# Optimization experiments

Measured on AMD Instinct MI355X. Metric: run time of the kernel, lower is better.

The kernel has to match this reference:

```python
import jax, jax.numpy as jnp
import numpy as np

N_HEADS, N_KV, HEAD_DIM = 16, 4, 64
DIM = 4096
LATENT = N_HEADS * HEAD_DIM   # 1024
KV_DIM = N_KV * HEAD_DIM      # 256
KSZ = 3


def _causal_conv1d(x, w, b, groups):
    # x: [B,S,C]; w: [Cout, Cin//groups, K]; causal left padding (K-1)
    y = jax.lax.conv_general_dilated(
        x.transpose(0, 2, 1), w, window_strides=(1,),
        padding=[(w.shape[-1] - 1, 0)], feature_group_count=groups,
        dimension_numbers=('NCH', 'OIH', 'NCH'))
    return (y + b[None, :, None]).transpose(0, 2, 1)


def _rope(x, cos, sin):
    # x: [B,H,S,D] interleaved pairs; cos/sin: [1,1,S,D//2]
    x1, x2 = x[..., ::2], x[..., 1::2]
    out = jnp.stack([x1 * cos - x2 * sin, x1 * sin + x2 * cos], axis=-1)
    return out.reshape(x.shape)


def _l2norm(x):
    n = jnp.sqrt(jnp.sum(x * x, axis=-1, keepdims=True))
    return x / jnp.maximum(n, 1e-12)


def setup_inputs() -> dict:
    key = jax.random.key(0)
    ks = jax.random.split(key, 12)
    sc = 0.02
    x = jax.random.normal(ks[0], (2, 2048, DIM), jnp.float32)
    w_qkv = jax.random.normal(ks[1], (LATENT + 2 * KV_DIM, DIM), jnp.float32) * sc
    w_o = jax.random.normal(ks[2], (DIM, LATENT), jnp.float32) * sc
    qc1_w = jax.random.normal(ks[3], (LATENT, LATENT // N_HEADS, KSZ), jnp.float32) * sc
    qc1_b = jnp.zeros((LATENT,), jnp.float32)
    qc2_w = jax.random.normal(ks[4], (LATENT, LATENT, KSZ), jnp.float32) * sc
    qc2_b = jnp.zeros((LATENT,), jnp.float32)
    kc1_w = jax.random.normal(ks[5], (KV_DIM, KV_DIM // N_KV, KSZ), jnp.float32) * sc
    kc1_b = jnp.zeros((KV_DIM,), jnp.float32)
    kc2_w = jax.random.normal(ks[6], (KV_DIM, KV_DIM, KSZ), jnp.float32) * sc
    kc2_b = jnp.zeros((KV_DIM,), jnp.float32)
    key_temp = jnp.full((1,), float(HEAD_DIM) ** 0.5, jnp.float32)
    return dict(x=x, w_qkv=w_qkv, w_o=w_o, qc1_w=qc1_w, qc1_b=qc1_b,
                qc2_w=qc2_w, qc2_b=qc2_b, kc1_w=kc1_w, kc1_b=kc1_b,
                kc2_w=kc2_w, kc2_b=kc2_b, key_temp=key_temp)


def _forward(x, w_qkv, w_o, qc1_w, qc1_b, qc2_w, qc2_b, kc1_w, kc1_b, kc2_w, kc2_b, key_temp):
    B, S, _ = x.shape
    qkv = x @ w_qkv.T  # [B,S,LATENT+2*KV_DIM]
    q = qkv[..., :LATENT]
    k = qkv[..., LATENT:LATENT + KV_DIM]
    # value shift: first half current token, second half previous token (0 at t=0)
    half = KV_DIM // 2
    v_curr = qkv[..., LATENT + KV_DIM:LATENT + KV_DIM + half]
    v_prev = qkv[..., LATENT + KV_DIM + half:]
    v = jnp.concatenate([v_curr, jnp.pad(v_prev[:, :-1, :], ((0, 0), (1, 0), (0, 0)))], axis=-1)
    q_pre, k_pre = q, k
    # grouped causal conv sequences on q and k
    q = _causal_conv1d(_causal_conv1d(q, qc1_w, qc1_b, N_HEADS), qc2_w, qc2_b, 1)
    k = _causal_conv1d(_causal_conv1d(k, kc1_w, kc1_b, N_KV), kc2_w, kc2_b, 1)
    # qk-mean coupling (n_groups = 4 branch)
    q_mean = q_pre.reshape(B, S, N_HEADS, HEAD_DIM).mean(axis=2)  # [B,S,hd]
    k_mean = k_pre.reshape(B, S, N_KV, HEAD_DIM).mean(axis=2)
    q = q.reshape(B, S, N_HEADS, HEAD_DIM) + 0.5 * k_mean[:, :, None, :]
    k = k.reshape(B, S, N_KV, HEAD_DIM) + 0.5 * q_mean[:, :, None, :]
    q = q.transpose(0, 2, 1, 3)                                   # [B,H,S,d]
    k = k.transpose(0, 2, 1, 3)                                   # [B,Hkv,S,d]
    v = v.reshape(B, S, N_KV, HEAD_DIM).transpose(0, 2, 1, 3)
    # qk-norm with learned key temperature
    q = _l2norm(q)
    k = _l2norm(k) * key_temp
    # RoPE (interleaved pairs)
    inv = 1.0 / (10000.0 ** (jnp.arange(0, HEAD_DIM, 2, dtype=jnp.float32) / HEAD_DIM))
    ang = jnp.arange(S, dtype=jnp.float32)[:, None] * inv[None, :]  # [S,d/2]
    cos, sin = jnp.cos(ang)[None, None], jnp.sin(ang)[None, None]
    q = _rope(q, cos, sin)
    k = _rope(k, cos, sin)
    # GQA: each kv head repeated n_groups times contiguously
    kg = jnp.repeat(k, N_HEADS // N_KV, axis=1)
    vg = jnp.repeat(v, N_HEADS // N_KV, axis=1)
    scale = HEAD_DIM ** -0.5
    scores = jnp.einsum('bhqd,bhkd->bhqk', q, kg) * scale
    causal = jnp.tril(jnp.ones((S, S), dtype=bool))
    scores = jnp.where(causal[None, None], scores, jnp.finfo(scores.dtype).min)
    attn = jax.nn.softmax(scores, axis=-1)
    out = jnp.einsum('bhqk,bhkd->bhqd', attn, vg)
    out = out.transpose(0, 2, 1, 3).reshape(B, S, LATENT)
    return out @ w_o.T  # output_scale = 1.0


def reference(x, w_qkv, w_o, qc1_w, qc1_b, qc2_w, qc2_b, kc1_w, kc1_b, kc2_w, kc2_b, key_temp):
    return _forward(x, w_qkv, w_o, qc1_w, qc1_b, qc2_w, qc2_b, kc1_w, kc1_b, kc2_w, kc2_b, key_temp)
```

## Files before the change

kernel.cpp:

```cpp
#include <hip/hip_runtime.h>
#include <hip/hip_bf16.h>
#include <cstddef>

#define NB 2
#define SEQ 2048
#define DIMX 4096
#define NH 16
#define NKV 4
#define HD 64
#define LATENT 1024
#define KVD 256
#define QKVN 1536
#define BS (NB*SEQ)
#define SP (SEQ+2)

typedef __attribute__((ext_vector_type(8))) short short8v;
typedef __attribute__((ext_vector_type(4))) float f32x4;
typedef __attribute__((ext_vector_type(4))) unsigned short ushort4v;
typedef __attribute__((ext_vector_type(4))) unsigned int uint4v;

static __device__ __forceinline__ unsigned short f2bf(float f) {
    union { float f; unsigned u; } v; v.f = f;
    unsigned r = v.u + 0x7fffu + ((v.u >> 16) & 1u);
    return (unsigned short)(r >> 16);
}

static __device__ __forceinline__ unsigned cvt_pk_bf16(float lo, float hi) {
    unsigned r;
    asm("v_cvt_pk_bf16_f32 %0, %1, %2" : "=v"(r) : "v"(lo), "v"(hi));
    return r;
}

static __device__ __forceinline__ void gload_lds16(const unsigned short* g, unsigned short* l) {
    __builtin_amdgcn_global_load_lds((const __attribute__((address_space(1))) void*)g,
                                     (__attribute__((address_space(3))) void*)l, 16, 0, 0);
}

__global__ __launch_bounds__(256)
void cast_f2b(const float* __restrict__ in, unsigned short* __restrict__ out, int n4)
{
    const int i = blockIdx.x * 256 + threadIdx.x;
    if (i < n4) {
        const float4 v = *reinterpret_cast<const float4*>(in + (size_t)i * 4);
        ushort4v o = {f2bf(v.x), f2bf(v.y), f2bf(v.z), f2bf(v.w)};
        *reinterpret_cast<ushort4v*>(out + (size_t)i * 4) = o;
    }
}

__global__ __launch_bounds__(256)
void w3reorder(const float* __restrict__ w, unsigned short* __restrict__ wr, int O, int I)
{
    const int idx = blockIdx.x * 256 + threadIdx.x;
    if (idx < O * I * 3) {
        const int o = idx / (I * 3), rem = idx % (I * 3);
        const int j = rem / I, c = rem % I;
        wr[idx] = f2bf(w[(size_t)o * I * 3 + c * 3 + j]);
    }
}

__global__ __launch_bounds__(256)
void zero_pad(unsigned short* __restrict__ pq, unsigned short* __restrict__ pk)
{
    const int t = blockIdx.x * 256 + threadIdx.x;
    if (t < 2 * 2 * LATENT) {
        const int b = t / (2 * LATENT), r = (t % (2 * LATENT)) / LATENT, c = t % LATENT;
        pq[((size_t)b * SP + r) * LATENT + c] = 0;
    }
    if (t < 2 * 2 * KVD) {
        const int b = t / (2 * KVD), r = (t % (2 * KVD)) / KVD, c = t % KVD;
        pk[((size_t)b * SP + r) * KVD + c] = 0;
    }
}

__global__ __launch_bounds__(256)
void rope_tab(float2* __restrict__ tab)
{
    const int idx = blockIdx.x * 256 + threadIdx.x;
    const int s = idx >> 5, i = idx & 31;
    const float inv = powf(10000.f, -(float)(2 * i) * (1.f / HD));
    const float ang = (float)s * inv;
    tab[idx] = make_float2(cosf(ang), sinf(ang));
}

template<int CONV>
__global__ __launch_bounds__(256)
void gemm_bf16(const unsigned short* __restrict__ A, const unsigned short* __restrict__ W,
               const float* __restrict__ bias, float* __restrict__ C,
               int M, int N, int K, int Cch, int klen, size_t pstride)
{
    __shared__ unsigned short Abuf[2][128 * 32];
    __shared__ unsigned short Bbuf[2][128 * 32];
    const int gx = gridDim.x;
    const int nwg = gx * gridDim.y;
    const int lin = blockIdx.y * gx + blockIdx.x;
    const int swz = (lin & 7) * (nwg >> 3) + (lin >> 3);
    const int n0 = (swz % gx) * 128, m0 = (swz / gx) * 128;
    const int koff = blockIdx.z * klen;
    C += (size_t)blockIdx.z * pstride;
    const int tid = threadIdx.x;
    const int wave = tid >> 6, lane = tid & 63;
    const int lg = lane >> 4, lr = lane & 15;
    const int wm = (wave & 1) * 64, wn = (wave >> 1) * 64;
    const int sr = wave * 32 + (lane >> 2);
    const int sc = (lane & 3) * 8;
    const int bb = m0 / SEQ, s0 = m0 % SEQ;

    const int NT = klen / 32;
    f32x4 acc[4][4];
    #pragma unroll
    for (int i = 0; i < 4; i++)
        #pragma unroll
        for (int j = 0; j < 4; j++) acc[i][j] = (f32x4){0.f, 0.f, 0.f, 0.f};

    auto stage = [&](int buf, int kt) {
        const int k0 = koff + kt * 32;
        const unsigned short* ga0;
        if (!CONV) {
            ga0 = A + (size_t)(m0 + sr) * K + k0 + sc;
        } else {
            const int j = k0 / Cch, c0 = k0 - j * Cch;
            ga0 = A + (size_t)(bb * SP + s0 + j + sr) * Cch + c0 + sc;
        }
        const unsigned short* gb0 = W + (size_t)(n0 + sr) * K + k0 + sc;
        const size_t astep = (size_t)16 * (CONV ? Cch : K);
        #pragma unroll
        for (int i = 0; i < 2; i++) {
            gload_lds16(ga0 + i * astep, &Abuf[buf][(wave * 2 + i) * 512]);
            gload_lds16(gb0 + (size_t)i * 16 * K, &Bbuf[buf][(wave * 2 + i) * 512]);
        }
    };

    stage(0, 0);
    __syncthreads();
    int cur = 0;
    for (int kt = 0; kt < NT; ++kt) {
        if (kt + 1 < NT) stage(cur ^ 1, kt + 1);
        short8v af[4], bf[4];
        #pragma unroll
        for (int mi = 0; mi < 4; mi++)
            af[mi] = *reinterpret_cast<const short8v*>(&Abuf[cur][(wm + mi * 16 + lr) * 32 + lg * 8]);
        #pragma unroll
        for (int ni = 0; ni < 4; ni++)
            bf[ni] = *reinterpret_cast<const short8v*>(&Bbuf[cur][(wn + ni * 16 + lr) * 32 + lg * 8]);
        #pragma unroll
        for (int mi = 0; mi < 4; mi++)
            #pragma unroll
            for (int ni = 0; ni < 4; ni++)
                acc[mi][ni] = __builtin_amdgcn_mfma_f32_16x16x32_bf16(af[mi], bf[ni], acc[mi][ni], 0, 0, 0);
        __syncthreads();
        cur ^= 1;
    }

    #pragma unroll
    for (int ni = 0; ni < 4; ni++) {
        const int col = n0 + wn + ni * 16 + lr;
        const float bv = bias ? bias[col] : 0.f;
        #pragma unroll
        for (int mi = 0; mi < 4; mi++)
            #pragma unroll
            for (int r = 0; r < 4; r++)
                C[(size_t)(m0 + wm + mi * 16 + lg * 4 + r) * N + col] = acc[mi][ni][r] + bv;
    }
}

__global__ __launch_bounds__(256)
void conv1_grouped(const float* __restrict__ qkv0, const float* __restrict__ qkv1, int coloff,
                   const float* __restrict__ w, const float* __restrict__ bias,
                   unsigned short* __restrict__ out, int CH)
{
    const int t0 = blockIdx.x * 64;
    const int b  = blockIdx.y;
    const int g  = blockIdx.z;
    __shared__ float xs[66][64];
    for (int idx = threadIdx.x; idx < 66 * 64; idx += 256) {
        const int i = idx >> 6, ic = idx & 63;
        const int tt = t0 + i - 2;
        float v = 0.f;
        if (tt >= 0) {
            const size_t off = (size_t)(b * SEQ + tt) * QKVN + coloff + g * 64 + ic;
            v = qkv0[off] + qkv1[off];
        }
        xs[i][ic] = v;
    }
    __syncthreads();
    const int oc = threadIdx.x & 63;
    const int ibase = (threadIdx.x >> 6) * 16;
    float acc[16];
    const float bv = bias[g * 64 + oc];
    #pragma unroll
    for (int i = 0; i < 16; i++) acc[i] = bv;
    const float* wp = w + (size_t)(g * 64 + oc) * 192;
    for (int ic = 0; ic < 64; ic++) {
        const float w0 = wp[ic * 3 + 0], w1 = wp[ic * 3 + 1], w2 = wp[ic * 3 + 2];
        float xv[18];
        #pragma unroll
        for (int r = 0; r < 18; r++) xv[r] = xs[ibase + r][ic];
        #pragma unroll
        for (int i = 0; i < 16; i++) acc[i] += w0 * xv[i] + w1 * xv[i + 1] + w2 * xv[i + 2];
    }
    #pragma unroll
    for (int i = 0; i < 16; i++)
        out[((size_t)b * SP + 2 + t0 + ibase + i) * CH + g * 64 + oc] = f2bf(acc[i]);
}

__global__ __launch_bounds__(64)
void meanv_kernel(const float* __restrict__ qkv0, const float* __restrict__ qkv1,
                  float* __restrict__ qmean, float* __restrict__ kmean,
                  unsigned short* __restrict__ vRow)
{
    const int t = blockIdx.x, d = threadIdx.x;
    const int b = t >> 11, s = t & (SEQ - 1);
    const float* r0 = qkv0 + (size_t)t * QKVN;
    const float* r1 = qkv1 + (size_t)t * QKVN;
    float qs = 0.f;
    #pragma unroll
    for (int h = 0; h < NH; h++) qs += r0[h * 64 + d] + r1[h * 64 + d];
    qmean[t * 64 + d] = qs * (1.f / NH);
    float ks = 0.f;
    #pragma unroll
    for (int h = 0; h < NKV; h++) ks += r0[LATENT + h * 64 + d] + r1[LATENT + h * 64 + d];
    kmean[t * 64 + d] = ks * (1.f / NKV);
    #pragma unroll
    for (int g = 0; g < NKV; g++) {
        const int c = g * 64 + d;
        float v;
        if (c < 128) {
            v = r0[LATENT + KVD + c] + r1[LATENT + KVD + c];
        } else {
            v = 0.f;
            if (s > 0) {
                const size_t off = (size_t)(t - 1) * QKVN + LATENT + KVD + 128 + (c - 128);
                v = qkv0[off] + qkv1[off];
            }
        }
        vRow[((size_t)(b * NKV + g) * SEQ + s) * 64 + d] = f2bf(v);
    }
}

__global__ __launch_bounds__(256)
void vtrans(const unsigned short* __restrict__ vRow, unsigned short* __restrict__ vTb)
{
    const int s0 = blockIdx.x * 64;
    const int bg = blockIdx.y;
    __shared__ unsigned short t[64][72];
    const int tid = threadIdx.x;
    {
        const int r = tid >> 2, c0 = (tid & 3) * 16;
        const unsigned short* p = vRow + ((size_t)bg * SEQ + s0 + r) * 64 + c0;
        const short8v a = *reinterpret_cast<const short8v*>(p);
        const short8v bv = *reinterpret_cast<const short8v*>(p + 8);
        #pragma unroll
        for (int j = 0; j < 8; j++) { t[r][c0 + j] = (unsigned short)a[j]; t[r][c0 + 8 + j] = (unsigned short)bv[j]; }
    }
    __syncthreads();
    {
        const int d = tid >> 2, ss = (tid & 3) * 16;
        short8v o0, o1;
        #pragma unroll
        for (int j = 0; j < 8; j++) { o0[j] = (short)t[ss + j][d]; o1[j] = (short)t[ss + 8 + j][d]; }
        unsigned short* op = vTb + ((size_t)bg * 64 + d) * SEQ + s0 + ss;
        *reinterpret_cast<short8v*>(op) = o0;
        *reinterpret_cast<short8v*>(op + 8) = o1;
    }
}

__global__ __launch_bounds__(64)
void qk_final(const float* __restrict__ qc2a, const float* __restrict__ qc2b,
              const float* __restrict__ kc2a, const float* __restrict__ kc2b,
              const float* __restrict__ qbias, const float* __restrict__ kbias,
              const float* __restrict__ qmean, const float* __restrict__ kmean,
              const float* __restrict__ key_temp, const float2* __restrict__ rtab,
              unsigned short* __restrict__ qTb, unsigned short* __restrict__ kTb)
{
    const int t = blockIdx.x, hh = blockIdx.y, d = threadIdx.x;
    const int b = t >> 11, s = t & (SEQ - 1);
    float val;
    if (hh < NH) {
        const size_t off = (size_t)t * LATENT + hh * 64 + d;
        val = qc2a[off] + qc2b[off] + qbias[hh * 64 + d] + 0.5f * kmean[t * 64 + d];
    } else {
        const size_t off = (size_t)t * KVD + (hh - NH) * 64 + d;
        val = kc2a[off] + kc2b[off] + kbias[(hh - NH) * 64 + d] + 0.5f * qmean[t * 64 + d];
    }
    float ss = val * val;
    #pragma unroll
    for (int off = 32; off >= 1; off >>= 1) ss += __shfl_xor(ss, off);
    const float n = sqrtf(ss);
    val = val / fmaxf(n, 1e-12f);
    if (hh >= NH) val *= key_temp[0];
    const float2 cs = rtab[s * 32 + (d >> 1)];
    const float cv = cs.x, sv = cs.y;
    const float partner = __shfl_xor(val, 1);
    const float x1 = (d & 1) ? partner : val;
    const float x2 = (d & 1) ? val : partner;
    const float o = (d & 1) ? (x1 * sv + x2 * cv) : (x1 * cv - x2 * sv);
    if (hh < NH) qTb[((size_t)(b * NH + hh) * SEQ + s) * 64 + d] = f2bf(o);
    else         kTb[((size_t)(b * NKV + (hh - NH)) * SEQ + s) * 64 + d] = f2bf(o);
}

__global__ __launch_bounds__(256)
void attn_mfma(const unsigned short* __restrict__ qTb, const unsigned short* __restrict__ kTb,
               const unsigned short* __restrict__ vTb, unsigned short* __restrict__ attn_out)
{
    const int wg = blockIdx.x;
    int bh, blk;
    if (wg < 256) {
        const int xcd = wg & 7, i = wg >> 3;
        bh = (xcd << 2) | (i >> 3);
        blk = 15 - (i & 7);
    } else {
        const int u = wg - 256;
        const int xcd = u & 7, i = u >> 3;
        bh = (xcd << 2) | (i >> 3);
        blk = i & 7;
    }
    const int b = bh >> 4, h = bh & 15, g = h >> 2;
    const int tid = threadIdx.x;
    const int wave = tid >> 6, lane = tid & 63;
    const int lg = lane >> 4, lr = lane & 15;
    const int qt = blk * 4 + wave;
    const int q0 = qt * 32;
    const int ctot2 = (blk + 1) * 2;

    __shared__ __align__(16) unsigned short SB[2][16][512];

    short8v qf[2][2];
    const unsigned short* qbase = qTb + ((size_t)(b * NH + h) * SEQ + q0) * 64;
    #pragma unroll
    for (int mf = 0; mf < 2; mf++)
        #pragma unroll
        for (int dc = 0; dc < 2; dc++)
            qf[mf][dc] = *reinterpret_cast<const short8v*>(qbase + (size_t)(mf * 16 + lr) * 64 + dc * 32 + lg * 8);

    f32x4 acc[2][4];
    float lsum[2] = {0.f, 0.f};
    #pragma unroll
    for (int mf = 0; mf < 2; mf++)
        #pragma unroll
        for (int dt = 0; dt < 4; dt++) acc[mf][dt] = (f32x4){0.f, 0.f, 0.f, 0.f};

    const unsigned short* kbase = kTb + (size_t)(b * NKV + g) * SEQ * 64;
    const unsigned short* vbase = vTb + (size_t)(b * NKV + g) * 64 * SEQ;
    const float EC = 0.125f * 1.44269504f;
    const int src01 = ((lg & 1) << 5) + lr;
    const int src23 = src01 + 16;
    const bool hi = (lg >= 2);

    auto stage64 = [&](int buf, int cc) {
        const int kb = cc * 64;
        #pragma unroll
        for (int i = 0; i < 4; i++) {
            const int ch = wave * 4 + i;
            const int st = ch >> 3, chl = ch & 7;
            const int k0 = kb + st * 32;
            const unsigned short* src;
            if (chl < 4) src = kbase + (size_t)(k0 + (chl >> 1) * 16 + lr) * 64 + (chl & 1) * 32 + lg * 8;
            else         src = vbase + (size_t)((chl - 4) * 16 + lr) * SEQ + k0 + lg * 8;
            gload_lds16(src, &SB[buf][ch][lane * 8]);
        }
    };

    stage64(0, 0);
    __syncthreads();
    int cur = 0;
    for (int cc = 0; cc < ctot2; ++cc) {
        if (cc + 1 < ctot2) stage64(cur ^ 1, cc + 1);
        #pragma unroll
        for (int st = 0; st < 2; ++st) {
            const int c = cc * 2 + st;
            if (c > qt) continue;
            const int k0 = c * 32;
            short8v kf[2][2], vf[4];
            #pragma unroll
            for (int kt = 0; kt < 2; kt++)
                #pragma unroll
                for (int dc = 0; dc < 2; dc++)
                    kf[kt][dc] = *reinterpret_cast<const short8v*>(&SB[cur][st * 8 + kt * 2 + dc][lane * 8]);
            #pragma unroll
            for (int dt = 0; dt < 4; dt++)
                vf[dt] = *reinterpret_cast<const short8v*>(&SB[cur][st * 8 + 4 + dt][lane * 8]);

            const bool diag = (c == qt);
            #pragma unroll
            for (int mf = 0; mf < 2; mf++) {
                f32x4 z0 = (f32x4){0.f, 0.f, 0.f, 0.f}, z1 = (f32x4){0.f, 0.f, 0.f, 0.f};
                __builtin_amdgcn_s_setprio(1);
                z0 = __builtin_amdgcn_mfma_f32_16x16x32_bf16(kf[0][0], qf[mf][0], z0, 0, 0, 0);
                z0 = __builtin_amdgcn_mfma_f32_16x16x32_bf16(kf[0][1], qf[mf][1], z0, 0, 0, 0);
                z1 = __builtin_amdgcn_mfma_f32_16x16x32_bf16(kf[1][0], qf[mf][0], z1, 0, 0, 0);
                z1 = __builtin_amdgcn_mfma_f32_16x16x32_bf16(kf[1][1], qf[mf][1], z1, 0, 0, 0);
                __builtin_amdgcn_s_setprio(0);
                float p0[4], p1[4];
                #pragma unroll
                for (int r = 0; r < 4; r++) {
                    p0[r] = exp2f(z0[r] * EC);
                    p1[r] = exp2f(z1[r] * EC);
                }
                if (diag) {
                    const int q = q0 + mf * 16 + lr;
                    #pragma unroll
                    for (int r = 0; r < 4; r++) {
                        if (k0 + 4 * lg + r > q)      p0[r] = 0.f;
                        if (k0 + 16 + 4 * lg + r > q) p1[r] = 0.f;
                    }
                }
                lsum[mf] += (p0[0] + p0[1]) + (p0[2] + p0[3]) + (p1[0] + p1[1]) + (p1[2] + p1[3]);
                const unsigned W00 = cvt_pk_bf16(p0[0], p0[1]);
                const unsigned W01 = cvt_pk_bf16(p0[2], p0[3]);
                const unsigned W10 = cvt_pk_bf16(p1[0], p1[1]);
                const unsigned W11 = cvt_pk_bf16(p1[2], p1[3]);
                const unsigned a0 = __shfl(W00, src01), b0 = __shfl(W10, src01);
                const unsigned a1 = __shfl(W01, src01), b1 = __shfl(W11, src01);
                const unsigned a2 = __shfl(W00, src23), b2 = __shfl(W10, src23);
                const unsigned a3 = __shfl(W01, src23), b3 = __shfl(W11, src23);
                uint4v pw;
                pw.x = hi ? b0 : a0;
                pw.y = hi ? b1 : a1;
                pw.z = hi ? b2 : a2;
                pw.w = hi ? b3 : a3;
                const short8v pa = __builtin_bit_cast(short8v, pw);
                __builtin_amdgcn_s_setprio(1);
                #pragma unroll
                for (int dt = 0; dt < 4; dt++)
                    acc[mf][dt] = __builtin_amdgcn_mfma_f32_16x16x32_bf16(pa, vf[dt], acc[mf][dt], 0, 0, 0);
                __builtin_amdgcn_s_setprio(0);
            }
        }
        __syncthreads();
        cur ^= 1;
    }

    float den[2];
    #pragma unroll
    for (int mf = 0; mf < 2; mf++) {
        float s = lsum[mf];
        s += __shfl_xor(s, 16); s += __shfl_xor(s, 32);
        den[mf] = s;
    }

    #pragma unroll
    for (int mf = 0; mf < 2; mf++) {
        float dinv[4];
        #pragma unroll
        for (int r = 0; r < 4; r++) dinv[r] = 1.f / __shfl(den[mf], 4 * lg + r);
        #pragma unroll
        for (int dt = 0; dt < 4; dt++)
            #pragma unroll
            for (int r = 0; r < 4; r++) {
                const int q = q0 + mf * 16 + 4 * lg + r;
                attn_out[(size_t)(b * SEQ + q) * LATENT + h * 64 + dt * 16 + lr] = f2bf(acc[mf][dt][r] * dinv[r]);
            }
    }
}

extern "C" void kernel_launch(void* const* d_in, const int* in_sizes, int n_in,
                              void* d_out, int out_size, void* d_ws, size_t ws_size,
                              hipStream_t stream)
{
    const float* x       = (const float*)d_in[0];
    const float* w_qkv   = (const float*)d_in[1];
    const float* w_o     = (const float*)d_in[2];
    const float* qc1_w   = (const float*)d_in[3];
    const float* qc1_b   = (const float*)d_in[4];
    const float* qc2_w   = (const float*)d_in[5];
    const float* qc2_b   = (const float*)d_in[6];
    const float* kc1_w   = (const float*)d_in[7];
    const float* kc1_b   = (const float*)d_in[8];
    const float* kc2_w   = (const float*)d_in[9];
    const float* kc2_b   = (const float*)d_in[10];
    const float* key_temp = (const float*)d_in[11];

    char* wsb = (char*)d_ws;
    float* qkv = (float*)wsb;                 wsb += (size_t)BS * QKVN * 4;
    float* qc2 = qkv;
    float* kc2 = (float*)((char*)qkv + (size_t)BS * LATENT * 4);
    unsigned short* pq  = (unsigned short*)wsb;  wsb += (size_t)NB * SP * LATENT * 2;
    unsigned short* pk  = (unsigned short*)wsb;  wsb += (size_t)NB * SP * KVD * 2;
    float* qmean = (float*)wsb;  wsb += (size_t)BS * HD * 4;
    float* kmean = (float*)wsb;  wsb += (size_t)BS * HD * 4;
    unsigned short* qTb  = (unsigned short*)wsb;  wsb += (size_t)BS * LATENT * 2;
    unsigned short* kTb  = (unsigned short*)wsb;  wsb += (size_t)BS * KVD * 2;
    unsigned short* vRow = (unsigned short*)wsb;  wsb += (size_t)BS * KVD * 2;
    unsigned short* vTb  = (unsigned short*)wsb;  wsb += (size_t)BS * KVD * 2;
    unsigned short* xb   = (unsigned short*)wsb;  wsb += (size_t)BS * DIMX * 2;
    unsigned short* attnb  = xb;
    unsigned short* qc2wr  = (unsigned short*)((char*)xb + (size_t)BS * LATENT * 2);
    unsigned short* kc2wr  = (unsigned short*)((char*)qc2wr + (size_t)LATENT * LATENT * 3 * 2);
    unsigned short* wqkvb = (unsigned short*)wsb;  wsb += (size_t)QKVN * DIMX * 2;
    unsigned short* wob   = wqkvb;

    float* outp = (float*)d_out;

    float* qkvp1 = outp;
    const size_t QKV_PS = (size_t)((ptrdiff_t)(qkvp1 - qkv));
    float* qc2p1 = (float*)((char*)d_ws + 67512320);
    float* kc2p1 = (float*)((char*)d_ws + (size_t)BS * QKVN * 4);
    const size_t QC2_PS = (size_t)(qc2p1 - qc2);
    const size_t KC2_PS = (size_t)(kc2p1 - kc2);
    float2* rtab = (float2*)vRow;

    cast_f2b<<<dim3(BS * DIMX / 4 / 256), 256, 0, stream>>>(x, xb, BS * DIMX / 4);
    cast_f2b<<<dim3(QKVN * DIMX / 4 / 256), 256, 0, stream>>>(w_qkv, wqkvb, QKVN * DIMX / 4);
    gemm_bf16<0><<<dim3(QKVN / 128, BS / 128, 2), 256, 0, stream>>>(xb, wqkvb, nullptr, qkv, BS, QKVN, DIMX, 0, DIMX / 2, QKV_PS);
    cast_f2b<<<dim3(DIMX * LATENT / 4 / 256), 256, 0, stream>>>(w_o, wob, DIMX * LATENT / 4);
    w3reorder<<<dim3((LATENT * LATENT * 3 + 255) / 256), 256, 0, stream>>>(qc2_w, qc2wr, LATENT, LATENT);
    w3reorder<<<dim3((KVD * KVD * 3 + 255) / 256), 256, 0, stream>>>(kc2_w, kc2wr, KVD, KVD);
    meanv_kernel<<<dim3(BS), 64, 0, stream>>>(qkv, qkvp1, qmean, kmean, vRow);
    vtrans<<<dim3(SEQ / 64, NB * NKV), 256, 0, stream>>>(vRow, vTb);
    rope_tab<<<dim3(SEQ * 32 / 256), 256, 0, stream>>>(rtab);
    zero_pad<<<dim3(16), 256, 0, stream>>>(pq, pk);
    conv1_grouped<<<dim3(SEQ / 64, NB, NH),  256, 0, stream>>>(qkv, qkvp1, 0,      qc1_w, qc1_b, pq, LATENT);
    conv1_grouped<<<dim3(SEQ / 64, NB, NKV), 256, 0, stream>>>(qkv, qkvp1, LATENT, kc1_w, kc1_b, pk, KVD);
    gemm_bf16<1><<<dim3(LATENT / 128, BS / 128, 2), 256, 0, stream>>>(pq, qc2wr, nullptr, qc2, BS, LATENT, LATENT * 3, LATENT, LATENT * 3 / 2, QC2_PS);
    gemm_bf16<1><<<dim3(KVD / 128, BS / 128, 2), 256, 0, stream>>>(pk, kc2wr, nullptr, kc2, BS, KVD, KVD * 3, KVD, KVD * 3 / 2, KC2_PS);
    qk_final<<<dim3(BS, NH + NKV), 64, 0, stream>>>(qc2, qc2p1, kc2, kc2p1, qc2_b, kc2_b,
                                                    qmean, kmean, key_temp, rtab, qTb, kTb);
    attn_mfma<<<dim3(512), 256, 0, stream>>>(qTb, kTb, vTb, attnb);
    gemm_bf16<0><<<dim3(DIMX / 128, BS / 128, 1), 256, 0, stream>>>(attnb, wob, nullptr, outp, BS, DIMX, LATENT, 0, LATENT, 0);
}
```

Measured before the change: 377.7 us.

## Split attention KV range in two with merge kernel; fuse prep kernels

The attention kernel now splits each query block's causal KV range into two halves handled by separate workgroups, doubling the grid to 1024. Each half writes unnormalized bf16 partial numerators and float denominators, and a new merge kernel sums and normalizes them. This relies on a fixed, non-max-subtracted softmax, so partials add directly. It also fuses the w_o cast, conv weight reorders, rope table and zero padding into one launch. The aim is better load balance and occupancy on attention and fewer launches, at the cost of extra partial-result traffic, a bf16 rounding step before the merge, and one more kernel.

```diff
diff --git a/kernel.cpp b/kernel.cpp
--- a/kernel.cpp
+++ b/kernel.cpp
@@ -47,39 +47,56 @@
     }
 }
 
-__global__ __launch_bounds__(256)
-void w3reorder(const float* __restrict__ w, unsigned short* __restrict__ wr, int O, int I)
-{
-    const int idx = blockIdx.x * 256 + threadIdx.x;
-    if (idx < O * I * 3) {
-        const int o = idx / (I * 3), rem = idx % (I * 3);
-        const int j = rem / I, c = rem % I;
-        wr[idx] = f2bf(w[(size_t)o * I * 3 + c * 3 + j]);
-    }
-}
-
-__global__ __launch_bounds__(256)
-void zero_pad(unsigned short* __restrict__ pq, unsigned short* __restrict__ pk)
-{
-    const int t = blockIdx.x * 256 + threadIdx.x;
-    if (t < 2 * 2 * LATENT) {
-        const int b = t / (2 * LATENT), r = (t % (2 * LATENT)) / LATENT, c = t % LATENT;
-        pq[((size_t)b * SP + r) * LATENT + c] = 0;
-    }
-    if (t < 2 * 2 * KVD) {
-        const int b = t / (2 * KVD), r = (t % (2 * KVD)) / KVD, c = t % KVD;
-        pk[((size_t)b * SP + r) * KVD + c] = 0;
-    }
-}
-
-__global__ __launch_bounds__(256)
-void rope_tab(float2* __restrict__ tab)
-{
-    const int idx = blockIdx.x * 256 + threadIdx.x;
-    const int s = idx >> 5, i = idx & 31;
-    const float inv = powf(10000.f, -(float)(2 * i) * (1.f / HD));
-    const float ang = (float)s * inv;
-    tab[idx] = make_float2(cosf(ang), sinf(ang));
+#define WO_BLK 4096
+#define QW_N (LATENT*LATENT*3)
+#define QW_BLK 12288
+#define KW_N (KVD*KVD*3)
+#define KW_BLK 768
+#define RT_BLK 256
+__global__ __launch_bounds__(256)
+void prep_misc(const float* __restrict__ wo, unsigned short* __restrict__ wob,
+               const float* __restrict__ qc2w, unsigned short* __restrict__ qc2wr,
+               const float* __restrict__ kc2w, unsigned short* __restrict__ kc2wr,
+               float2* __restrict__ rtab,
+               unsigned short* __restrict__ pq, unsigned short* __restrict__ pk)
+{
+    const int blk = blockIdx.x, tid = threadIdx.x;
+    if (blk < WO_BLK) {
+        const int i = blk * 256 + tid;
+        const float4 v = *reinterpret_cast<const float4*>(wo + (size_t)i * 4);
+        ushort4v o = {f2bf(v.x), f2bf(v.y), f2bf(v.z), f2bf(v.w)};
+        *reinterpret_cast<ushort4v*>(wob + (size_t)i * 4) = o;
+    } else if (blk < WO_BLK + QW_BLK) {
+        const int idx = (blk - WO_BLK) * 256 + tid;
+        if (idx < QW_N) {
+            const int o = idx / (LATENT * 3), rem = idx % (LATENT * 3);
+            const int j = rem / LATENT, c = rem % LATENT;
+            qc2wr[idx] = f2bf(qc2w[(size_t)o * LATENT * 3 + c * 3 + j]);
+        }
+    } else if (blk < WO_BLK + QW_BLK + KW_BLK) {
+        const int idx = (blk - WO_BLK - QW_BLK) * 256 + tid;
+        if (idx < KW_N) {
+            const int o = idx / (KVD * 3), rem = idx % (KVD * 3);
+            const int j = rem / KVD, c = rem % KVD;
+            kc2wr[idx] = f2bf(kc2w[(size_t)o * KVD * 3 + c * 3 + j]);
+        }
+    } else if (blk < WO_BLK + QW_BLK + KW_BLK + RT_BLK) {
+        const int idx = (blk - WO_BLK - QW_BLK - KW_BLK) * 256 + tid;
+        const int s = idx >> 5, i = idx & 31;
+        const float inv = powf(10000.f, -(float)(2 * i) * (1.f / HD));
+        const float ang = (float)s * inv;
+        rtab[idx] = make_float2(cosf(ang), sinf(ang));
+    } else {
+        const int t = (blk - WO_BLK - QW_BLK - KW_BLK - RT_BLK) * 256 + tid;
+        if (t < 2 * 2 * LATENT) {
+            const int b = t / (2 * LATENT), r = (t % (2 * LATENT)) / LATENT, c = t % LATENT;
+            pq[((size_t)b * SP + r) * LATENT + c] = 0;
+        }
+        if (t < 2 * 2 * KVD) {
+            const int b = t / (2 * KVD), r = (t % (2 * KVD)) / KVD, c = t % KVD;
+            pk[((size_t)b * SP + r) * KVD + c] = 0;
+        }
+    }
 }
 
 template<int CONV>
@@ -300,27 +317,27 @@
 
 __global__ __launch_bounds__(256)
 void attn_mfma(const unsigned short* __restrict__ qTb, const unsigned short* __restrict__ kTb,
-               const unsigned short* __restrict__ vTb, unsigned short* __restrict__ attn_out)
+               const unsigned short* __restrict__ vTb,
+               unsigned short* __restrict__ pnum, float* __restrict__ pden)
 {
     const int wg = blockIdx.x;
-    int bh, blk;
-    if (wg < 256) {
-        const int xcd = wg & 7, i = wg >> 3;
-        bh = (xcd << 2) | (i >> 3);
-        blk = 15 - (i & 7);
-    } else {
-        const int u = wg - 256;
-        const int xcd = u & 7, i = u >> 3;
-        bh = (xcd << 2) | (i >> 3);
-        blk = i & 7;
-    }
+    const int qg = wg >> 8;
+    const int u = wg & 255;
+    const int xcd = u & 7, i = u >> 3;
+    const int bh = (xcd << 2) | (i >> 3);
+    const int r = i & 7;
+    const int p = (qg == 0) ? r : (qg == 1) ? (15 - r) : (qg == 2) ? (16 + r) : (31 - r);
+    const int blk = 15 - (p >> 1);
+    const int part = p & 1;
+    const int half = blk + 1;
+    const int cbeg = part * half, cend = cbeg + half;
+
     const int b = bh >> 4, h = bh & 15, g = h >> 2;
     const int tid = threadIdx.x;
     const int wave = tid >> 6, lane = tid & 63;
     const int lg = lane >> 4, lr = lane & 15;
     const int qt = blk * 4 + wave;
     const int q0 = qt * 32;
-    const int ctot2 = (blk + 1) * 2;
 
     __shared__ __align__(16) unsigned short SB[2][16][512];
 
@@ -349,8 +366,8 @@
     auto stage64 = [&](int buf, int cc) {
         const int kb = cc * 64;
         #pragma unroll
-        for (int i = 0; i < 4; i++) {
-            const int ch = wave * 4 + i;
+        for (int i2 = 0; i2 < 4; i2++) {
+            const int ch = wave * 4 + i2;
             const int st = ch >> 3, chl = ch & 7;
             const int k0 = kb + st * 32;
             const unsigned short* src;
@@ -360,11 +377,11 @@
         }
     };
 
-    stage64(0, 0);
+    stage64(0, cbeg);
     __syncthreads();
     int cur = 0;
-    for (int cc = 0; cc < ctot2; ++cc) {
-        if (cc + 1 < ctot2) stage64(cur ^ 1, cc + 1);
+    for (int cc = cbeg; cc < cend; ++cc) {
+        if (cc + 1 < cend) stage64(cur ^ 1, cc + 1);
         #pragma unroll
         for (int st = 0; st < 2; ++st) {
             const int c = cc * 2 + st;
@@ -392,16 +409,16 @@
                 __builtin_amdgcn_s_setprio(0);
                 float p0[4], p1[4];
                 #pragma unroll
-                for (int r = 0; r < 4; r++) {
-                    p0[r] = exp2f(z0[r] * EC);
-                    p1[r] = exp2f(z1[r] * EC);
+                for (int rr = 0; rr < 4; rr++) {
+                    p0[rr] = exp2f(z0[rr] * EC);
+                    p1[rr] = exp2f(z1[rr] * EC);
                 }
                 if (diag) {
                     const int q = q0 + mf * 16 + lr;
                     #pragma unroll
-                    for (int r = 0; r < 4; r++) {
-                        if (k0 + 4 * lg + r > q)      p0[r] = 0.f;
-                        if (k0 + 16 + 4 * lg + r > q) p1[r] = 0.f;
+                    for (int rr = 0; rr < 4; rr++) {
+                        if (k0 + 4 * lg + rr > q)      p0[rr] = 0.f;
+                        if (k0 + 16 + 4 * lg + rr > q) p1[rr] = 0.f;
                     }
                 }
                 lsum[mf] += (p0[0] + p0[1]) + (p0[2] + p0[3]) + (p1[0] + p1[1]) + (p1[2] + p1[3]);
@@ -438,19 +455,46 @@
         den[mf] = s;
     }
 
-    #pragma unroll
-    for (int mf = 0; mf < 2; mf++) {
-        float dinv[4];
-        #pragma unroll
-        for (int r = 0; r < 4; r++) dinv[r] = 1.f / __shfl(den[mf], 4 * lg + r);
+    const int base = ((bh * 64 + qt) * 2 + part);
+    if (lg == 0) {
+        pden[base * 32 + lr] = den[0];
+        pden[base * 32 + 16 + lr] = den[1];
+    }
+    unsigned short* np = pnum + (size_t)base * 2048;
+    #pragma unroll
+    for (int mf = 0; mf < 2; mf++)
         #pragma unroll
         for (int dt = 0; dt < 4; dt++)
             #pragma unroll
-            for (int r = 0; r < 4; r++) {
-                const int q = q0 + mf * 16 + 4 * lg + r;
-                attn_out[(size_t)(b * SEQ + q) * LATENT + h * 64 + dt * 16 + lr] = f2bf(acc[mf][dt][r] * dinv[r]);
-            }
-    }
+            for (int rr = 0; rr < 4; rr++)
+                np[(mf * 16 + 4 * lg + rr) * 64 + dt * 16 + lr] = f2bf(acc[mf][dt][rr]);
+}
+
+__global__ __launch_bounds__(256)
+void attn_merge(const unsigned short* __restrict__ pnum, const float* __restrict__ pden,
+                unsigned short* __restrict__ attnb)
+{
+    const int idx = blockIdx.x * 256 + threadIdx.x;
+    const int d0 = (idx & 7) * 8;
+    const int qr = (idx >> 3) & 31;
+    const int qt = (idx >> 8) & 63;
+    const int bh = idx >> 14;
+    const int base = (bh * 64 + qt) * 2;
+    const float den = pden[base * 32 + qr] + pden[(base + 1) * 32 + qr];
+    const float inv = 1.f / den;
+    const short8v n0 = *reinterpret_cast<const short8v*>(pnum + (size_t)base * 2048 + qr * 64 + d0);
+    const short8v n1 = *reinterpret_cast<const short8v*>(pnum + (size_t)(base + 1) * 2048 + qr * 64 + d0);
+    short8v ov;
+    #pragma unroll
+    for (int j = 0; j < 8; j++) {
+        union { unsigned u; float f; } t0, t1;
+        t0.u = ((unsigned)(unsigned short)n0[j]) << 16;
+        t1.u = ((unsigned)(unsigned short)n1[j]) << 16;
+        ov[j] = (short)f2bf((t0.f + t1.f) * inv);
+    }
+    const int q = qt * 32 + qr;
+    const int b = bh >> 4, h = bh & 15;
+    *reinterpret_cast<short8v*>(attnb + (size_t)(b * SEQ + q) * LATENT + h * 64 + d0) = ov;
 }
 
 extern "C" void kernel_launch(void* const* d_in, const int* in_sizes, int n_in,
@@ -497,24 +541,24 @@
     float* kc2p1 = (float*)((char*)d_ws + (size_t)BS * QKVN * 4);
     const size_t QC2_PS = (size_t)(qc2p1 - qc2);
     const size_t KC2_PS = (size_t)(kc2p1 - kc2);
-    float2* rtab = (float2*)vRow;
+    float2* rtab = (float2*)((char*)d_ws + 84289536);
+    unsigned short* apnum = (unsigned short*)d_ws;
+    float* apden = (float*)((char*)d_ws + 16777216);
 
     cast_f2b<<<dim3(BS * DIMX / 4 / 256), 256, 0, stream>>>(x, xb, BS * DIMX / 4);
     cast_f2b<<<dim3(QKVN * DIMX / 4 / 256), 256, 0, stream>>>(w_qkv, wqkvb, QKVN * DIMX / 4);
     gemm_bf16<0><<<dim3(QKVN / 128, BS / 128, 2), 256, 0, stream>>>(xb, wqkvb, nullptr, qkv, BS, QKVN, DIMX, 0, DIMX / 2, QKV_PS);
-    cast_f2b<<<dim3(DIMX * LATENT / 4 / 256), 256, 0, stream>>>(w_o, wob, DIMX * LATENT / 4);
-    w3reorder<<<dim3((LATENT * LATENT * 3 + 255) / 256), 256, 0, stream>>>(qc2_w, qc2wr, LATENT, LATENT);
-    w3reorder<<<dim3((KVD * KVD * 3 + 255) / 256), 256, 0, stream>>>(kc2_w, kc2wr, KVD, KVD);
+    prep_misc<<<dim3(WO_BLK + QW_BLK + KW_BLK + RT_BLK + 16), 256, 0, stream>>>(
+        w_o, wob, qc2_w, qc2wr, kc2_w, kc2wr, rtab, pq, pk);
     meanv_kernel<<<dim3(BS), 64, 0, stream>>>(qkv, qkvp1, qmean, kmean, vRow);
     vtrans<<<dim3(SEQ / 64, NB * NKV), 256, 0, stream>>>(vRow, vTb);
-    rope_tab<<<dim3(SEQ * 32 / 256), 256, 0, stream>>>(rtab);
-    zero_pad<<<dim3(16), 256, 0, stream>>>(pq, pk);
     conv1_grouped<<<dim3(SEQ / 64, NB, NH),  256, 0, stream>>>(qkv, qkvp1, 0,      qc1_w, qc1_b, pq, LATENT);
     conv1_grouped<<<dim3(SEQ / 64, NB, NKV), 256, 0, stream>>>(qkv, qkvp1, LATENT, kc1_w, kc1_b, pk, KVD);
     gemm_bf16<1><<<dim3(LATENT / 128, BS / 128, 2), 256, 0, stream>>>(pq, qc2wr, nullptr, qc2, BS, LATENT, LATENT * 3, LATENT, LATENT * 3 / 2, QC2_PS);
     gemm_bf16<1><<<dim3(KVD / 128, BS / 128, 2), 256, 0, stream>>>(pk, kc2wr, nullptr, kc2, BS, KVD, KVD * 3, KVD, KVD * 3 / 2, KC2_PS);
     qk_final<<<dim3(BS, NH + NKV), 64, 0, stream>>>(qc2, qc2p1, kc2, kc2p1, qc2_b, kc2_b,
                                                     qmean, kmean, key_temp, rtab, qTb, kTb);
-    attn_mfma<<<dim3(512), 256, 0, stream>>>(qTb, kTb, vTb, attnb);
+    attn_mfma<<<dim3(1024), 256, 0, stream>>>(qTb, kTb, vTb, apnum, apden);
+    attn_merge<<<dim3(2048), 256, 0, stream>>>(apnum, apden, attnb);
     gemm_bf16<0><<<dim3(DIMX / 128, BS / 128, 1), 256, 0, stream>>>(attnb, wob, nullptr, outp, BS, DIMX, LATENT, 0, LATENT, 0);
 }
```

Measured after the change: 356.4 us. 1.06x faster.
